# Kernel optimization log

Measured on AMD Instinct MI355X. Metric: run time of the kernel, lower is better.

The kernel has to match this reference:

```python
import jax, jax.numpy as jnp
import numpy as np

B, N, DIM = 4, 2048, 512
HEADS, DK = 8, 64
SCALE = DK ** -0.5


def setup_inputs() -> dict:
    key = jax.random.key(0)
    k1, k2, k3, k4 = jax.random.split(key, 4)
    x = jax.random.normal(k1, (B, N, DIM), dtype=jnp.float32)
    # nn.Linear(dim, dim_key*heads, bias=False): y = x @ W.T; store W already transposed
    Wq = jax.random.normal(k2, (DIM, HEADS * DK), dtype=jnp.float32) * (DIM ** -0.5)
    Wk = jax.random.normal(k3, (DIM, HEADS * DK), dtype=jnp.float32) * (DIM ** -0.5)
    rel_content_bias = jax.random.normal(k4, (1, HEADS, 1, DK), dtype=jnp.float32)
    return {"x": x, "Wq": Wq, "Wk": Wk, "rel_content_bias": rel_content_bias}


def _split_heads(t, h):
    # [b, n, h*d] -> [b, h, n, d]
    b, n, hd = t.shape
    return t.reshape(b, n, h, hd // h).transpose(0, 2, 1, 3)


def reference(x, Wq, Wk, rel_content_bias):
    q = _split_heads(x @ Wq, HEADS) * SCALE          # [b, h, n, dk]
    k = _split_heads(x @ Wk, HEADS)                  # [b, h, n, dk]
    v = _split_heads(x, HEADS)                       # [b, h, n, dim/h]
    logits = jnp.einsum('bhid,bhjd->bhij', q + rel_content_bias, k)
    attn = jax.nn.sigmoid(logits)                    # no softmax normalization
    out = jnp.einsum('bhij,bhjd->bhid', attn, v)     # [b, h, n, dim/h]
    b, h, n, d = out.shape
    return out.transpose(0, 2, 1, 3).reshape(b, n, h * d)
```

## Files before the change

### kernel.cpp

```cpp
#include <hip/hip_runtime.h>
#include <hip/hip_bf16.h>
#include <stdint.h>

#define BB 4
#define NN 2048
#define DIMD 512
#define HH 8
#define DKK 64
#define MTOT (BB * NN)
constexpr float SCALE = 0.125f;

typedef __attribute__((ext_vector_type(4))) float f32x4;
typedef __attribute__((ext_vector_type(2))) float f32x2;
typedef __attribute__((ext_vector_type(8))) short bf16x8;
typedef __attribute__((ext_vector_type(4))) _Float16 f16x4;
typedef __attribute__((ext_vector_type(2))) __fp16 fp16v2;
typedef __attribute__((ext_vector_type(4))) __fp16 fp16v4;
typedef __attribute__((ext_vector_type(2))) unsigned int u32x2;

union pack8 { unsigned short s[8]; uint4 v; };
union fragu { u32x2 h[2]; bf16x8 v; };

__device__ __forceinline__ unsigned short f2bf(float f) {
  union { float f; uint32_t u; } v; v.f = f;
  uint32_t u = v.u;
  return (unsigned short)((u + 0x7FFFu + ((u >> 16) & 1u)) >> 16);
}

__device__ __forceinline__ unsigned short f2h(float f) {
  union { _Float16 h; unsigned short u; } c; c.h = (_Float16)f;
  return c.u;
}

__device__ __forceinline__ bf16x8 ld_frag(const unsigned short* p) {
  fragu f;
  f.h[0] = *(const u32x2*)p;
  f.h[1] = *(const u32x2*)(p + 4);
  return f.v;
}
__device__ __forceinline__ void st8(unsigned short* p, uint4 v) {
  *(u32x2*)p = (u32x2){v.x, v.y};
  *(u32x2*)(p + 4) = (u32x2){v.z, v.w};
}

__device__ __forceinline__ f16x4 sig_pack(f32x4 sv) {
  float e0 = __expf(-__builtin_fabsf(sv[0]));
  float e1 = __expf(-__builtin_fabsf(sv[1]));
  float e2 = __expf(-__builtin_fabsf(sv[2]));
  float e3 = __expf(-__builtin_fabsf(sv[3]));
  const f32x2 c3 = {-0.22184f, -0.22184f};
  const f32x2 c2 = {0.66550f, 0.66550f};
  const f32x2 c1 = {-0.94280f, -0.94280f};
  const f32x2 c0 = {0.49826f, 0.49826f};
  f32x2 eA = {e0, e1}, eB = {e2, e3};
  f32x2 pA = __builtin_elementwise_fma(
      __builtin_elementwise_fma(__builtin_elementwise_fma(c3, eA, c2), eA, c1),
      eA, c0);
  f32x2 pB = __builtin_elementwise_fma(
      __builtin_elementwise_fma(__builtin_elementwise_fma(c3, eB, c2), eB, c1),
      eB, c0);
  float r0 = __builtin_copysignf(pA.x, sv[0]) + 0.5f;
  float r1 = __builtin_copysignf(pA.y, sv[1]) + 0.5f;
  float r2 = __builtin_copysignf(pB.x, sv[2]) + 0.5f;
  float r3 = __builtin_copysignf(pB.y, sv[3]) + 0.5f;
  fp16v2 lo = __builtin_amdgcn_cvt_pkrtz(r0, r1);
  fp16v2 hi = __builtin_amdgcn_cvt_pkrtz(r2, r3);
  fp16v4 p;
  p.x = lo.x; p.y = lo.y; p.z = hi.x; p.w = hi.y;
  return __builtin_bit_cast(f16x4, p);
}

__global__ __launch_bounds__(256) void prep(const float* __restrict__ x,
                                            const float* __restrict__ wq,
                                            const float* __restrict__ wk,
                                            unsigned short* __restrict__ xb,
                                            unsigned short* __restrict__ xtf,
                                            unsigned short* __restrict__ wtq,
                                            unsigned short* __restrict__ wtk) {
  const int bx = blockIdx.x, tid = threadIdx.x;
  if (bx < 2048) {
    size_t base = ((size_t)bx * 256 + tid) * 8;
    float4 a = *(const float4*)(x + base);
    float4 b = *(const float4*)(x + base + 4);
    pack8 p;
    p.s[0] = f2bf(a.x); p.s[1] = f2bf(a.y); p.s[2] = f2bf(a.z); p.s[3] = f2bf(a.w);
    p.s[4] = f2bf(b.x); p.s[5] = f2bf(b.y); p.s[6] = f2bf(b.z); p.s[7] = f2bf(b.w);
    *(uint4*)(xb + base) = p.v;
  } else if (bx < 2304) {
    int q = bx - 2048;
    int b = q >> 6, r = q & 63;
    int dt = r >> 3, nt = r & 7;
    int d = dt * 64 + (tid & 63);
    int n0 = nt * 256 + (tid >> 6) * 64;
    const float* xp = x + ((size_t)b * NN + n0) * DIMD + d;
    unsigned short* dp = xtf + ((size_t)b * DIMD + d) * NN + n0;
#pragma unroll
    for (int g = 0; g < 8; g++) {
      pack8 pa;
#pragma unroll
      for (int k = 0; k < 8; k++) pa.s[k] = f2h(xp[(size_t)(g * 8 + k) * DIMD]);
      *(uint4*)(dp + g * 8) = pa.v;
    }
  } else {
    __shared__ __align__(16) unsigned short T[64][68];
    int q = bx - 2304;
    const float* w = (q >= 64) ? wk : wq;
    unsigned short* wt = (q >= 64) ? wtk : wtq;
    int r = q & 63;
    int kt = r >> 3, nt = r & 7;
    const int k0 = kt * 64, n0 = nt * 64;
#pragma unroll
    for (int rr = 0; rr < 16; rr++) {
      int idx = tid + rr * 256;
      int kl = idx >> 6, nl = idx & 63;
      T[nl][kl] = f2bf(w[(size_t)(k0 + kl) * DIMD + n0 + nl]);
    }
    __syncthreads();
#pragma unroll
    for (int rr = 0; rr < 2; rr++) {
      int idx = tid + rr * 256;
      int nl = idx >> 3, c = idx & 7;
      fragu f;
      f.h[0] = *(const u32x2*)&T[nl][c * 8];
      f.h[1] = *(const u32x2*)&T[nl][c * 8 + 4];
      uint4 v;
      v.x = f.h[0].x; v.y = f.h[0].y; v.z = f.h[1].x; v.w = f.h[1].y;
      *(uint4*)(wt + (size_t)(n0 + nl) * DIMD + k0 + c * 8) = v;
    }
  }
}

__global__ __launch_bounds__(512, 4) void qk_gemm(const unsigned short* __restrict__ xb,
                                                  const unsigned short* __restrict__ wtq,
                                                  const unsigned short* __restrict__ wtk,
                                                  const float* __restrict__ bias,
                                                  unsigned short* __restrict__ qout,
                                                  unsigned short* __restrict__ kout) {
  __shared__ __align__(16) unsigned short Als[128][68];
  __shared__ __align__(16) unsigned short Bls[128][68];
  const int mb = blockIdx.x, nb = blockIdx.y;
  const bool isQ = (nb < 4);
  const unsigned short* wt = isQ ? wtq : wtk;
  unsigned short* outp = isQ ? qout : kout;
  const int n0 = (nb & 3) * 128, m0 = mb * 128;
  const int tid = threadIdx.x;
  const int wave = tid >> 6, lane = tid & 63;
  const int quad = lane >> 4, l16 = lane & 15;
  const int wm = wave >> 2, wn = wave & 3;

  f32x4 acc[4][2];
#pragma unroll
  for (int a = 0; a < 4; a++)
#pragma unroll
    for (int c = 0; c < 2; c++) acc[a][c] = (f32x4){0.f, 0.f, 0.f, 0.f};

  const int srow[2] = {tid >> 3, (tid + 512) >> 3};
  const int scol = (tid & 7) * 8;
  uint4 pa[2], pb[2];
#pragma unroll
  for (int r = 0; r < 2; r++) {
    pa[r] = *(const uint4*)(xb + (size_t)(m0 + srow[r]) * DIMD + scol);
    pb[r] = *(const uint4*)(wt + (size_t)(n0 + srow[r]) * DIMD + scol);
  }

  for (int k0 = 0; k0 < DIMD; k0 += 64) {
    __syncthreads();
#pragma unroll
    for (int r = 0; r < 2; r++) {
      st8(&Als[srow[r]][scol], pa[r]);
      st8(&Bls[srow[r]][scol], pb[r]);
    }
    __syncthreads();
    if (k0 + 64 < DIMD) {
#pragma unroll
      for (int r = 0; r < 2; r++) {
        pa[r] = *(const uint4*)(xb + (size_t)(m0 + srow[r]) * DIMD + k0 + 64 + scol);
        pb[r] = *(const uint4*)(wt + (size_t)(n0 + srow[r]) * DIMD + k0 + 64 + scol);
      }
    }
#pragma unroll
    for (int ks = 0; ks < 2; ks++) {
      bf16x8 af[4], bfr[2];
#pragma unroll
      for (int t = 0; t < 4; t++)
        af[t] = ld_frag(&Als[wm * 64 + t * 16 + l16][quad * 8 + ks * 32]);
#pragma unroll
      for (int t = 0; t < 2; t++)
        bfr[t] = ld_frag(&Bls[wn * 32 + t * 16 + l16][quad * 8 + ks * 32]);
#pragma unroll
      for (int tm = 0; tm < 4; tm++)
#pragma unroll
        for (int tn = 0; tn < 2; tn++)
          acc[tm][tn] =
              __builtin_amdgcn_mfma_f32_16x16x32_bf16(af[tm], bfr[tn], acc[tm][tn], 0, 0, 0);
    }
  }
#pragma unroll
  for (int tm = 0; tm < 4; tm++) {
#pragma unroll
    for (int tn = 0; tn < 2; tn++) {
#pragma unroll
      for (int r = 0; r < 4; r++) {
        int row = m0 + wm * 64 + tm * 16 + quad * 4 + r;
        int gcol = n0 + wn * 32 + tn * 16 + l16;
        float v = acc[tm][tn][r];
        if (isQ) v = v * SCALE + bias[gcol];
        outp[(size_t)row * DIMD + gcol] = f2bf(v);
      }
    }
  }
}

__global__ __launch_bounds__(512, 4) void attn(const unsigned short* __restrict__ qb,
                                               const unsigned short* __restrict__ kb,
                                               const unsigned short* __restrict__ xtf,
                                               float* __restrict__ out) {
  __shared__ __align__(16) char smem[34816];
  unsigned short* Kall = (unsigned short*)smem;
  unsigned short* Vall = Kall + 2 * 64 * 68;
  float* R0 = (float*)smem;

  const int it = blockIdx.x, bh = blockIdx.y;
  const int b = bh >> 3, h = bh & 7;
  const int i0 = it * 128;
  const int tid = threadIdx.x;
  const int lane = tid & 63;
  const int grp = tid >> 8;
  const int wv = (tid >> 6) & 3;
  const int gtid = tid & 255;
  const int quad = lane >> 4, l16 = lane & 15;

  bf16x8 qf[2][2];
  int irow[2];
#pragma unroll
  for (int s_ = 0; s_ < 2; s_++) {
    irow[s_] = i0 + wv * 32 + s_ * 16 + l16;
    const unsigned short* qp = qb + ((size_t)b * NN + irow[s_]) * DIMD + h * DKK + quad * 8;
    qf[s_][0] = *(const bf16x8*)qp;
    qf[s_][1] = *(const bf16x8*)(qp + 32);
  }

  f32x4 o[2][4];
#pragma unroll
  for (int s_ = 0; s_ < 2; s_++)
#pragma unroll
    for (int td = 0; td < 4; td++) o[s_][td] = (f32x4){0.f, 0.f, 0.f, 0.f};

  const unsigned short* kbase = kb + (size_t)b * NN * DIMD + h * DKK;
  const unsigned short* vbase = xtf + ((size_t)b * DIMD + h * DKK) * NN;
  unsigned short* Kg = Kall + grp * (64 * 68);
  unsigned short* Vg = Vall + grp * (64 * 68);
  const int jbase = grp * 1024;

  const int trow[2] = {gtid >> 3, (gtid + 256) >> 3};
  const int tcol = (gtid & 7) * 8;
  uint4 pk[2], pv[2];
#pragma unroll
  for (int r = 0; r < 2; r++) {
    pk[r] = *(const uint4*)(kbase + (size_t)(jbase + trow[r]) * DIMD + tcol);
    pv[r] = *(const uint4*)(vbase + (size_t)trow[r] * NN + jbase + tcol);
  }

  for (int itr = 0; itr < 16; itr++) {
    __syncthreads();
#pragma unroll
    for (int r = 0; r < 2; r++) {
      st8(&Kg[trow[r] * 68 + tcol], pk[r]);
      st8(&Vg[trow[r] * 68 + tcol], pv[r]);
    }
    __syncthreads();
    if (itr < 15) {
      const int j0 = jbase + (itr + 1) * 64;
#pragma unroll
      for (int r = 0; r < 2; r++) {
        pk[r] = *(const uint4*)(kbase + (size_t)(j0 + trow[r]) * DIMD + tcol);
        pv[r] = *(const uint4*)(vbase + (size_t)trow[r] * NN + j0 + tcol);
      }
    }

#pragma unroll
    for (int t = 0; t < 4; t++) {
      bf16x8 kf0 = ld_frag(&Kg[(t * 16 + l16) * 68 + quad * 8]);
      bf16x8 kf1 = ld_frag(&Kg[(t * 16 + l16) * 68 + quad * 8 + 32]);
      f16x4 pf[2];
#pragma unroll
      for (int s_ = 0; s_ < 2; s_++) {
        f32x4 sv = (f32x4){0.f, 0.f, 0.f, 0.f};
        sv = __builtin_amdgcn_mfma_f32_16x16x32_bf16(kf0, qf[s_][0], sv, 0, 0, 0);
        sv = __builtin_amdgcn_mfma_f32_16x16x32_bf16(kf1, qf[s_][1], sv, 0, 0, 0);
        pf[s_] = sig_pack(sv);
      }
#pragma unroll
      for (int td = 0; td < 4; td++) {
        f16x4 vf = __builtin_bit_cast(
            f16x4, *(const u32x2*)&Vg[(td * 16 + l16) * 68 + t * 16 + quad * 4]);
        o[0][td] = __builtin_amdgcn_mfma_f32_16x16x16f16(vf, pf[0], o[0][td], 0, 0, 0);
        o[1][td] = __builtin_amdgcn_mfma_f32_16x16x16f16(vf, pf[1], o[1][td], 0, 0, 0);
      }
    }
  }

  __syncthreads();
  if (grp == 1) {
#pragma unroll
    for (int s_ = 0; s_ < 2; s_++)
#pragma unroll
      for (int td = 0; td < 4; td++) {
        int base = (wv * 32 + s_ * 16 + l16) * 66 + td * 16 + quad * 4;
        *(f32x2*)&R0[base] = (f32x2){o[s_][td][0], o[s_][td][1]};
        *(f32x2*)&R0[base + 2] = (f32x2){o[s_][td][2], o[s_][td][3]};
      }
  }
  __syncthreads();
  if (grp == 0) {
#pragma unroll
    for (int s_ = 0; s_ < 2; s_++) {
#pragma unroll
      for (int td = 0; td < 4; td++) {
        int base = (wv * 32 + s_ * 16 + l16) * 66 + td * 16 + quad * 4;
        f32x2 a = *(const f32x2*)&R0[base];
        f32x2 c = *(const f32x2*)&R0[base + 2];
        o[s_][td][0] += a.x; o[s_][td][1] += a.y;
        o[s_][td][2] += c.x; o[s_][td][3] += c.y;
        float* op = out + ((size_t)b * NN + irow[s_]) * DIMD + h * DKK + td * 16 + quad * 4;
        *(f32x4*)op = o[s_][td];
      }
    }
  }
}

extern "C" void kernel_launch(void* const* d_in, const int* in_sizes, int n_in,
                              void* d_out, int out_size, void* d_ws, size_t ws_size,
                              hipStream_t stream) {
  const float* x = (const float*)d_in[0];
  const float* Wq = (const float*)d_in[1];
  const float* Wk = (const float*)d_in[2];
  const float* bias = (const float*)d_in[3];
  float* out = (float*)d_out;

  unsigned short* ws = (unsigned short*)d_ws;
  unsigned short* xb = ws;
  unsigned short* xtf = xb + (size_t)MTOT * DIMD;
  unsigned short* wtq = xtf + (size_t)MTOT * DIMD;
  unsigned short* wtk = wtq + (size_t)DIMD * DIMD;
  unsigned short* qb = wtk + (size_t)DIMD * DIMD;
  unsigned short* kb = qb + (size_t)MTOT * DIMD;

  prep<<<dim3(2432), 256, 0, stream>>>(x, Wq, Wk, xb, xtf, wtq, wtk);
  qk_gemm<<<dim3(64, 8), 512, 0, stream>>>(xb, wtq, wtk, bias, qb, kb);
  attn<<<dim3(16, 32), 512, 0, stream>>>(qb, kb, xtf, out);
}
```

Measured before the change: 158.5 us.

## Factor sigmoid constant term into column sums and shrink attention/GEMM tiles

The 0.5 offset is removed from the polynomial sigmoid, so the attention MFMA accumulates only the odd part. The missing 0.5·sum_j V[j] term is added once per output element from per-batch column sums of x, which prep computes with atomics into a buffer zeroed by an added memset. It also halves the row tile of qk_gemm and attn, doubling grid sizes and raising launch-bounds occupancy to 8 waves per SIMD. The cost is an extra memset launch, atomics in prep, and half the per-block data reuse of the K/V tiles loaded into shared memory.

```diff
diff --git a/kernel.cpp b/kernel.cpp
--- a/kernel.cpp
+++ b/kernel.cpp
@@ -59,10 +59,10 @@
   f32x2 pB = __builtin_elementwise_fma(
       __builtin_elementwise_fma(__builtin_elementwise_fma(c3, eB, c2), eB, c1),
       eB, c0);
-  float r0 = __builtin_copysignf(pA.x, sv[0]) + 0.5f;
-  float r1 = __builtin_copysignf(pA.y, sv[1]) + 0.5f;
-  float r2 = __builtin_copysignf(pB.x, sv[2]) + 0.5f;
-  float r3 = __builtin_copysignf(pB.y, sv[3]) + 0.5f;
+  float r0 = __builtin_copysignf(pA.x, sv[0]);
+  float r1 = __builtin_copysignf(pA.y, sv[1]);
+  float r2 = __builtin_copysignf(pB.x, sv[2]);
+  float r3 = __builtin_copysignf(pB.y, sv[3]);
   fp16v2 lo = __builtin_amdgcn_cvt_pkrtz(r0, r1);
   fp16v2 hi = __builtin_amdgcn_cvt_pkrtz(r2, r3);
   fp16v4 p;
@@ -76,7 +76,8 @@
                                             unsigned short* __restrict__ xb,
                                             unsigned short* __restrict__ xtf,
                                             unsigned short* __restrict__ wtq,
-                                            unsigned short* __restrict__ wtk) {
+                                            unsigned short* __restrict__ wtk,
+                                            float* __restrict__ vsum) {
   const int bx = blockIdx.x, tid = threadIdx.x;
   if (bx < 2048) {
     size_t base = ((size_t)bx * 256 + tid) * 8;
@@ -94,13 +95,19 @@
     int n0 = nt * 256 + (tid >> 6) * 64;
     const float* xp = x + ((size_t)b * NN + n0) * DIMD + d;
     unsigned short* dp = xtf + ((size_t)b * DIMD + d) * NN + n0;
+    float s = 0.f;
 #pragma unroll
     for (int g = 0; g < 8; g++) {
       pack8 pa;
 #pragma unroll
-      for (int k = 0; k < 8; k++) pa.s[k] = f2h(xp[(size_t)(g * 8 + k) * DIMD]);
+      for (int k = 0; k < 8; k++) {
+        float v = xp[(size_t)(g * 8 + k) * DIMD];
+        s += v;
+        pa.s[k] = f2h(v);
+      }
       *(uint4*)(dp + g * 8) = pa.v;
     }
+    atomicAdd(&vsum[(size_t)b * DIMD + d], s);
   } else {
     __shared__ __align__(16) unsigned short T[64][68];
     int q = bx - 2304;
@@ -130,65 +137,62 @@
   }
 }
 
-__global__ __launch_bounds__(512, 4) void qk_gemm(const unsigned short* __restrict__ xb,
+__global__ __launch_bounds__(512, 8) void qk_gemm(const unsigned short* __restrict__ xb,
                                                   const unsigned short* __restrict__ wtq,
                                                   const unsigned short* __restrict__ wtk,
                                                   const float* __restrict__ bias,
                                                   unsigned short* __restrict__ qout,
                                                   unsigned short* __restrict__ kout) {
-  __shared__ __align__(16) unsigned short Als[128][68];
+  __shared__ __align__(16) unsigned short Als[64][68];
   __shared__ __align__(16) unsigned short Bls[128][68];
   const int mb = blockIdx.x, nb = blockIdx.y;
   const bool isQ = (nb < 4);
   const unsigned short* wt = isQ ? wtq : wtk;
   unsigned short* outp = isQ ? qout : kout;
-  const int n0 = (nb & 3) * 128, m0 = mb * 128;
+  const int n0 = (nb & 3) * 128, m0 = mb * 64;
   const int tid = threadIdx.x;
   const int wave = tid >> 6, lane = tid & 63;
   const int quad = lane >> 4, l16 = lane & 15;
   const int wm = wave >> 2, wn = wave & 3;
 
-  f32x4 acc[4][2];
-#pragma unroll
-  for (int a = 0; a < 4; a++)
+  f32x4 acc[2][2];
+#pragma unroll
+  for (int a = 0; a < 2; a++)
 #pragma unroll
     for (int c = 0; c < 2; c++) acc[a][c] = (f32x4){0.f, 0.f, 0.f, 0.f};
 
-  const int srow[2] = {tid >> 3, (tid + 512) >> 3};
+  const int srowA = tid >> 3;
+  const int srowB[2] = {tid >> 3, (tid + 512) >> 3};
   const int scol = (tid & 7) * 8;
-  uint4 pa[2], pb[2];
-#pragma unroll
-  for (int r = 0; r < 2; r++) {
-    pa[r] = *(const uint4*)(xb + (size_t)(m0 + srow[r]) * DIMD + scol);
-    pb[r] = *(const uint4*)(wt + (size_t)(n0 + srow[r]) * DIMD + scol);
-  }
+  uint4 pa, pb[2];
+  pa = *(const uint4*)(xb + (size_t)(m0 + srowA) * DIMD + scol);
+#pragma unroll
+  for (int r = 0; r < 2; r++)
+    pb[r] = *(const uint4*)(wt + (size_t)(n0 + srowB[r]) * DIMD + scol);
 
   for (int k0 = 0; k0 < DIMD; k0 += 64) {
     __syncthreads();
-#pragma unroll
-    for (int r = 0; r < 2; r++) {
-      st8(&Als[srow[r]][scol], pa[r]);
-      st8(&Bls[srow[r]][scol], pb[r]);
-    }
+    st8(&Als[srowA][scol], pa);
+    st8(&Bls[srowB[0]][scol], pb[0]);
+    st8(&Bls[srowB[1]][scol], pb[1]);
     __syncthreads();
     if (k0 + 64 < DIMD) {
-#pragma unroll
-      for (int r = 0; r < 2; r++) {
-        pa[r] = *(const uint4*)(xb + (size_t)(m0 + srow[r]) * DIMD + k0 + 64 + scol);
-        pb[r] = *(const uint4*)(wt + (size_t)(n0 + srow[r]) * DIMD + k0 + 64 + scol);
-      }
+      pa = *(const uint4*)(xb + (size_t)(m0 + srowA) * DIMD + k0 + 64 + scol);
+#pragma unroll
+      for (int r = 0; r < 2; r++)
+        pb[r] = *(const uint4*)(wt + (size_t)(n0 + srowB[r]) * DIMD + k0 + 64 + scol);
     }
 #pragma unroll
     for (int ks = 0; ks < 2; ks++) {
-      bf16x8 af[4], bfr[2];
-#pragma unroll
-      for (int t = 0; t < 4; t++)
-        af[t] = ld_frag(&Als[wm * 64 + t * 16 + l16][quad * 8 + ks * 32]);
+      bf16x8 af[2], bfr[2];
+#pragma unroll
+      for (int t = 0; t < 2; t++)
+        af[t] = ld_frag(&Als[wm * 32 + t * 16 + l16][quad * 8 + ks * 32]);
 #pragma unroll
       for (int t = 0; t < 2; t++)
         bfr[t] = ld_frag(&Bls[wn * 32 + t * 16 + l16][quad * 8 + ks * 32]);
 #pragma unroll
-      for (int tm = 0; tm < 4; tm++)
+      for (int tm = 0; tm < 2; tm++)
 #pragma unroll
         for (int tn = 0; tn < 2; tn++)
           acc[tm][tn] =
@@ -196,12 +200,12 @@
     }
   }
 #pragma unroll
-  for (int tm = 0; tm < 4; tm++) {
+  for (int tm = 0; tm < 2; tm++) {
 #pragma unroll
     for (int tn = 0; tn < 2; tn++) {
 #pragma unroll
       for (int r = 0; r < 4; r++) {
-        int row = m0 + wm * 64 + tm * 16 + quad * 4 + r;
+        int row = m0 + wm * 32 + tm * 16 + quad * 4 + r;
         int gcol = n0 + wn * 32 + tn * 16 + l16;
         float v = acc[tm][tn][r];
         if (isQ) v = v * SCALE + bias[gcol];
@@ -211,9 +215,10 @@
   }
 }
 
-__global__ __launch_bounds__(512, 4) void attn(const unsigned short* __restrict__ qb,
+__global__ __launch_bounds__(512, 8) void attn(const unsigned short* __restrict__ qb,
                                                const unsigned short* __restrict__ kb,
                                                const unsigned short* __restrict__ xtf,
+                                               const float* __restrict__ vsum,
                                                float* __restrict__ out) {
   __shared__ __align__(16) char smem[34816];
   unsigned short* Kall = (unsigned short*)smem;
@@ -222,7 +227,7 @@
 
   const int it = blockIdx.x, bh = blockIdx.y;
   const int b = bh >> 3, h = bh & 7;
-  const int i0 = it * 128;
+  const int i0 = it * 64;
   const int tid = threadIdx.x;
   const int lane = tid & 63;
   const int grp = tid >> 8;
@@ -230,21 +235,14 @@
   const int gtid = tid & 255;
   const int quad = lane >> 4, l16 = lane & 15;
 
-  bf16x8 qf[2][2];
-  int irow[2];
-#pragma unroll
-  for (int s_ = 0; s_ < 2; s_++) {
-    irow[s_] = i0 + wv * 32 + s_ * 16 + l16;
-    const unsigned short* qp = qb + ((size_t)b * NN + irow[s_]) * DIMD + h * DKK + quad * 8;
-    qf[s_][0] = *(const bf16x8*)qp;
-    qf[s_][1] = *(const bf16x8*)(qp + 32);
-  }
-
-  f32x4 o[2][4];
-#pragma unroll
-  for (int s_ = 0; s_ < 2; s_++)
-#pragma unroll
-    for (int td = 0; td < 4; td++) o[s_][td] = (f32x4){0.f, 0.f, 0.f, 0.f};
+  const int irow = i0 + wv * 16 + l16;
+  const unsigned short* qp = qb + ((size_t)b * NN + irow) * DIMD + h * DKK + quad * 8;
+  bf16x8 qf0 = *(const bf16x8*)qp;
+  bf16x8 qf1 = *(const bf16x8*)(qp + 32);
+
+  f32x4 o[4];
+#pragma unroll
+  for (int td = 0; td < 4; td++) o[td] = (f32x4){0.f, 0.f, 0.f, 0.f};
 
   const unsigned short* kbase = kb + (size_t)b * NN * DIMD + h * DKK;
   const unsigned short* vbase = xtf + ((size_t)b * DIMD + h * DKK) * NN;
@@ -282,20 +280,15 @@
     for (int t = 0; t < 4; t++) {
       bf16x8 kf0 = ld_frag(&Kg[(t * 16 + l16) * 68 + quad * 8]);
       bf16x8 kf1 = ld_frag(&Kg[(t * 16 + l16) * 68 + quad * 8 + 32]);
-      f16x4 pf[2];
-#pragma unroll
-      for (int s_ = 0; s_ < 2; s_++) {
-        f32x4 sv = (f32x4){0.f, 0.f, 0.f, 0.f};
-        sv = __builtin_amdgcn_mfma_f32_16x16x32_bf16(kf0, qf[s_][0], sv, 0, 0, 0);
-        sv = __builtin_amdgcn_mfma_f32_16x16x32_bf16(kf1, qf[s_][1], sv, 0, 0, 0);
-        pf[s_] = sig_pack(sv);
-      }
+      f32x4 sv = (f32x4){0.f, 0.f, 0.f, 0.f};
+      sv = __builtin_amdgcn_mfma_f32_16x16x32_bf16(kf0, qf0, sv, 0, 0, 0);
+      sv = __builtin_amdgcn_mfma_f32_16x16x32_bf16(kf1, qf1, sv, 0, 0, 0);
+      f16x4 pf = sig_pack(sv);
 #pragma unroll
       for (int td = 0; td < 4; td++) {
         f16x4 vf = __builtin_bit_cast(
             f16x4, *(const u32x2*)&Vg[(td * 16 + l16) * 68 + t * 16 + quad * 4]);
-        o[0][td] = __builtin_amdgcn_mfma_f32_16x16x16f16(vf, pf[0], o[0][td], 0, 0, 0);
-        o[1][td] = __builtin_amdgcn_mfma_f32_16x16x16f16(vf, pf[1], o[1][td], 0, 0, 0);
+        o[td] = __builtin_amdgcn_mfma_f32_16x16x16f16(vf, pf, o[td], 0, 0, 0);
       }
     }
   }
@@ -303,28 +296,26 @@
   __syncthreads();
   if (grp == 1) {
 #pragma unroll
-    for (int s_ = 0; s_ < 2; s_++)
-#pragma unroll
-      for (int td = 0; td < 4; td++) {
-        int base = (wv * 32 + s_ * 16 + l16) * 66 + td * 16 + quad * 4;
-        *(f32x2*)&R0[base] = (f32x2){o[s_][td][0], o[s_][td][1]};
-        *(f32x2*)&R0[base + 2] = (f32x2){o[s_][td][2], o[s_][td][3]};
-      }
+    for (int td = 0; td < 4; td++) {
+      int base = (wv * 16 + l16) * 66 + td * 16 + quad * 4;
+      *(f32x2*)&R0[base] = (f32x2){o[td][0], o[td][1]};
+      *(f32x2*)&R0[base + 2] = (f32x2){o[td][2], o[td][3]};
+    }
   }
   __syncthreads();
   if (grp == 0) {
 #pragma unroll
-    for (int s_ = 0; s_ < 2; s_++) {
-#pragma unroll
-      for (int td = 0; td < 4; td++) {
-        int base = (wv * 32 + s_ * 16 + l16) * 66 + td * 16 + quad * 4;
-        f32x2 a = *(const f32x2*)&R0[base];
-        f32x2 c = *(const f32x2*)&R0[base + 2];
-        o[s_][td][0] += a.x; o[s_][td][1] += a.y;
-        o[s_][td][2] += c.x; o[s_][td][3] += c.y;
-        float* op = out + ((size_t)b * NN + irow[s_]) * DIMD + h * DKK + td * 16 + quad * 4;
-        *(f32x4*)op = o[s_][td];
-      }
+    for (int td = 0; td < 4; td++) {
+      int base = (wv * 16 + l16) * 66 + td * 16 + quad * 4;
+      f32x2 a = *(const f32x2*)&R0[base];
+      f32x2 c = *(const f32x2*)&R0[base + 2];
+      f32x4 vs = *(const f32x4*)&vsum[(size_t)b * DIMD + h * DKK + td * 16 + quad * 4];
+      o[td][0] += a.x + 0.5f * vs[0];
+      o[td][1] += a.y + 0.5f * vs[1];
+      o[td][2] += c.x + 0.5f * vs[2];
+      o[td][3] += c.y + 0.5f * vs[3];
+      float* op = out + ((size_t)b * NN + irow) * DIMD + h * DKK + td * 16 + quad * 4;
+      *(f32x4*)op = o[td];
     }
   }
 }
@@ -345,8 +336,10 @@
   unsigned short* wtk = wtq + (size_t)DIMD * DIMD;
   unsigned short* qb = wtk + (size_t)DIMD * DIMD;
   unsigned short* kb = qb + (size_t)MTOT * DIMD;
-
-  prep<<<dim3(2432), 256, 0, stream>>>(x, Wq, Wk, xb, xtf, wtq, wtk);
-  qk_gemm<<<dim3(64, 8), 512, 0, stream>>>(xb, wtq, wtk, bias, qb, kb);
-  attn<<<dim3(16, 32), 512, 0, stream>>>(qb, kb, xtf, out);
-}
+  float* vsum = (float*)(kb + (size_t)MTOT * DIMD);
+
+  hipMemsetAsync(vsum, 0, (size_t)BB * DIMD * sizeof(float), stream);
+  prep<<<dim3(2432), 256, 0, stream>>>(x, Wq, Wk, xb, xtf, wtq, wtk, vsum);
+  qk_gemm<<<dim3(128, 8), 512, 0, stream>>>(xb, wtq, wtk, bias, qb, kb);
+  attn<<<dim3(32, 32), 512, 0, stream>>>(qb, kb, xtf, vsum, out);
+}
```

After: 174.1 us. 9.8% more time.

## Factor sigmoid constant half into precomputed column sums of V

Applied to the files above, without the earlier changes.

The 0.5 offset is dropped from the per-element sigmoid approximation, so each element now goes through an odd polynomial only. The removed constant is restored at the end by adding 0.5 times the column sum of V, which the transpose stage of the prep kernel accumulates with atomics. The attention grid is also swapped so consecutive blocks share a row tile across heads, and the MFMA loop is wrapped in s_setprio to raise wave priority. This adds a memset, atomics and an extra buffer, and it changes the fp16 rounding of P slightly by centring values around zero.

```diff
diff --git a/kernel.cpp b/kernel.cpp
--- a/kernel.cpp
+++ b/kernel.cpp
@@ -59,10 +59,10 @@
   f32x2 pB = __builtin_elementwise_fma(
       __builtin_elementwise_fma(__builtin_elementwise_fma(c3, eB, c2), eB, c1),
       eB, c0);
-  float r0 = __builtin_copysignf(pA.x, sv[0]) + 0.5f;
-  float r1 = __builtin_copysignf(pA.y, sv[1]) + 0.5f;
-  float r2 = __builtin_copysignf(pB.x, sv[2]) + 0.5f;
-  float r3 = __builtin_copysignf(pB.y, sv[3]) + 0.5f;
+  float r0 = __builtin_copysignf(pA.x, sv[0]);
+  float r1 = __builtin_copysignf(pA.y, sv[1]);
+  float r2 = __builtin_copysignf(pB.x, sv[2]);
+  float r3 = __builtin_copysignf(pB.y, sv[3]);
   fp16v2 lo = __builtin_amdgcn_cvt_pkrtz(r0, r1);
   fp16v2 hi = __builtin_amdgcn_cvt_pkrtz(r2, r3);
   fp16v4 p;
@@ -76,7 +76,8 @@
                                             unsigned short* __restrict__ xb,
                                             unsigned short* __restrict__ xtf,
                                             unsigned short* __restrict__ wtq,
-                                            unsigned short* __restrict__ wtk) {
+                                            unsigned short* __restrict__ wtk,
+                                            float* __restrict__ vsum) {
   const int bx = blockIdx.x, tid = threadIdx.x;
   if (bx < 2048) {
     size_t base = ((size_t)bx * 256 + tid) * 8;
@@ -94,13 +95,19 @@
     int n0 = nt * 256 + (tid >> 6) * 64;
     const float* xp = x + ((size_t)b * NN + n0) * DIMD + d;
     unsigned short* dp = xtf + ((size_t)b * DIMD + d) * NN + n0;
+    float s = 0.f;
 #pragma unroll
     for (int g = 0; g < 8; g++) {
       pack8 pa;
 #pragma unroll
-      for (int k = 0; k < 8; k++) pa.s[k] = f2h(xp[(size_t)(g * 8 + k) * DIMD]);
+      for (int k = 0; k < 8; k++) {
+        float v = xp[(size_t)(g * 8 + k) * DIMD];
+        s += v;
+        pa.s[k] = f2h(v);
+      }
       *(uint4*)(dp + g * 8) = pa.v;
     }
+    atomicAdd(&vsum[(size_t)b * DIMD + d], s);
   } else {
     __shared__ __align__(16) unsigned short T[64][68];
     int q = bx - 2304;
@@ -214,13 +221,14 @@
 __global__ __launch_bounds__(512, 4) void attn(const unsigned short* __restrict__ qb,
                                                const unsigned short* __restrict__ kb,
                                                const unsigned short* __restrict__ xtf,
+                                               const float* __restrict__ vsum,
                                                float* __restrict__ out) {
   __shared__ __align__(16) char smem[34816];
   unsigned short* Kall = (unsigned short*)smem;
   unsigned short* Vall = Kall + 2 * 64 * 68;
   float* R0 = (float*)smem;
 
-  const int it = blockIdx.x, bh = blockIdx.y;
+  const int bh = blockIdx.x, it = blockIdx.y;
   const int b = bh >> 3, h = bh & 7;
   const int i0 = it * 128;
   const int tid = threadIdx.x;
@@ -278,6 +286,7 @@
       }
     }
 
+    __builtin_amdgcn_s_setprio(1);
 #pragma unroll
     for (int t = 0; t < 4; t++) {
       bf16x8 kf0 = ld_frag(&Kg[(t * 16 + l16) * 68 + quad * 8]);
@@ -298,6 +307,7 @@
         o[1][td] = __builtin_amdgcn_mfma_f32_16x16x16f16(vf, pf[1], o[1][td], 0, 0, 0);
       }
     }
+    __builtin_amdgcn_s_setprio(0);
   }
 
   __syncthreads();
@@ -313,6 +323,7 @@
   }
   __syncthreads();
   if (grp == 0) {
+    const float* vsbase = vsum + (size_t)b * DIMD + h * DKK;
 #pragma unroll
     for (int s_ = 0; s_ < 2; s_++) {
 #pragma unroll
@@ -320,8 +331,11 @@
         int base = (wv * 32 + s_ * 16 + l16) * 66 + td * 16 + quad * 4;
         f32x2 a = *(const f32x2*)&R0[base];
         f32x2 c = *(const f32x2*)&R0[base + 2];
-        o[s_][td][0] += a.x; o[s_][td][1] += a.y;
-        o[s_][td][2] += c.x; o[s_][td][3] += c.y;
+        f32x4 vs = *(const f32x4*)&vsbase[td * 16 + quad * 4];
+        o[s_][td][0] += a.x + 0.5f * vs[0];
+        o[s_][td][1] += a.y + 0.5f * vs[1];
+        o[s_][td][2] += c.x + 0.5f * vs[2];
+        o[s_][td][3] += c.y + 0.5f * vs[3];
         float* op = out + ((size_t)b * NN + irow[s_]) * DIMD + h * DKK + td * 16 + quad * 4;
         *(f32x4*)op = o[s_][td];
       }
@@ -345,8 +359,10 @@
   unsigned short* wtk = wtq + (size_t)DIMD * DIMD;
   unsigned short* qb = wtk + (size_t)DIMD * DIMD;
   unsigned short* kb = qb + (size_t)MTOT * DIMD;
-
-  prep<<<dim3(2432), 256, 0, stream>>>(x, Wq, Wk, xb, xtf, wtq, wtk);
+  float* vsum = (float*)(kb + (size_t)MTOT * DIMD);
+
+  hipMemsetAsync(vsum, 0, (size_t)BB * DIMD * sizeof(float), stream);
+  prep<<<dim3(2432), 256, 0, stream>>>(x, Wq, Wk, xb, xtf, wtq, wtk, vsum);
   qk_gemm<<<dim3(64, 8), 512, 0, stream>>>(xb, wtq, wtk, bias, qb, kb);
-  attn<<<dim3(16, 32), 512, 0, stream>>>(qb, kb, xtf, out);
-}
+  attn<<<dim3(32, 16), 512, 0, stream>>>(qb, kb, xtf, vsum, out);
+}
```

Result: no change. 159.8 us (+0.8%).
